# Performance work log

Hardware: AMD Instinct MI355X
Metric: run time of the kernel (lower is better)

## Reference

```python
import jax, jax.numpy as jnp
import numpy as np
from jax import lax

FIELD = 32          # backbone receptive-field stride (field_size of ResNet50)
K = 3               # number of anchor sizes
ANCHOR_PX = (32, 64, 96)
POOL = 2
TILES = 3
NMS_IOU = 0.3
R_POST = 512        # post-NMS proposal cap (static shape for jit)
IMG = 1536
MG = IMG // FIELD   # 48x48 feature map
C = 256
HID = 1024


def setup_inputs() -> dict:
    key = jax.random.key(0)
    ks = jax.random.split(key, 6)
    # create_anchors: per feature cell (grid step FIELD) and per anchor size,
    # row = [x_upper_left, y_upper_left, width, height]
    grid = np.arange(MG, dtype=np.float32) * FIELD + FIELD / 2.0  # cell centers
    cy, cx, aa = np.meshgrid(grid, grid, np.array(ANCHOR_PX, np.float32), indexing='ij')
    anchors = np.stack([cx - aa / 2, cy - aa / 2, aa, aa], axis=-1).reshape(-1, 4).astype(np.float32)
    return {
        'features': jax.random.normal(ks[0], (1, MG, MG, C), jnp.float32),
        'anchors': jnp.asarray(anchors),
        'W_obj': jax.random.normal(ks[1], (C, 2 * K), jnp.float32) * 0.1,
        'b_obj': jnp.zeros((2 * K,), jnp.float32),
        'W_reg': jax.random.normal(ks[2], (C, 4 * K), jnp.float32) * 0.01,
        'b_reg': jnp.zeros((4 * K,), jnp.float32),
        'W_fc1': jax.random.normal(ks[3], (TILES * TILES * C, HID), jnp.float32) * 0.02,
        'b_fc1': jnp.zeros((HID,), jnp.float32),
        'W_fc2': jax.random.normal(ks[4], (HID, 4), jnp.float32) * 0.01,
        'b_fc2': jnp.zeros((4,), jnp.float32),
    }


def _map_outputs(out, anchors):
    # out: [M, N, K*D] RPN output; returns [A, D], one row per anchor
    apx = jnp.asarray(ANCHOR_PX, jnp.int32)
    k = jnp.argmax(anchors[:, 3].astype(jnp.int32)[:, None] == apx[None, :], axis=1)
    px = ((anchors[:, 0] + anchors[:, 2] * 0.5) / FIELD).astype(jnp.int32)
    py = ((anchors[:, 1] + anchors[:, 3] * 0.5) / FIELD).astype(jnp.int32)
    M, N, _ = out.shape
    r = out.reshape(M, N, K, -1)
    return r[py, px, k]


def _unparameterize(reg, anchors):
    cxa = anchors[:, 0] + anchors[:, 2] * 0.5
    cya = anchors[:, 1] + anchors[:, 3] * 0.5
    cx = reg[:, 0] * anchors[:, 2] + cxa
    cy = reg[:, 1] * anchors[:, 3] + cya
    w = anchors[:, 2] * jnp.exp(reg[:, 2])
    h = anchors[:, 3] * jnp.exp(reg[:, 3])
    return jnp.stack([cx - w * 0.5, cy - h * 0.5, w, h], axis=1)


def _clip_boxes(b, W, H):
    x1 = jnp.clip(b[:, 0], 0.0, W)
    y1 = jnp.clip(b[:, 1], 0.0, H)
    x2 = jnp.clip(b[:, 0] + b[:, 2], 0.0, W)
    y2 = jnp.clip(b[:, 1] + b[:, 3], 0.0, H)
    return jnp.stack([x1, y1, x2 - x1, y2 - y1], axis=1)


def _pairwise_iou(b):
    x1, y1 = b[:, 0], b[:, 1]
    x2, y2 = b[:, 0] + b[:, 2], b[:, 1] + b[:, 3]
    iw = jnp.maximum(0.0, jnp.minimum(x2[:, None], x2[None, :]) - jnp.maximum(x1[:, None], x1[None, :]))
    ih = jnp.maximum(0.0, jnp.minimum(y2[:, None], y2[None, :]) - jnp.maximum(y1[:, None], y1[None, :]))
    inter = iw * ih
    area = (x2 - x1) * (y2 - y1)
    return inter / (area[:, None] + area[None, :] - inter + 1e-8)


def _roialign(fmap, boxes):
    # fmap: [M, N, C]; boxes: [R, 4] xywh -> [R, TILES, TILES, C]
    M, N, Cc = fmap.shape
    S = TILES * POOL
    offs = (jnp.arange(S, dtype=boxes.dtype) + 0.5) / S
    fx = jnp.clip((boxes[:, 0:1] + offs[None, :] * boxes[:, 2:3]) / FIELD - 0.5, 0.0, N - 1.0)
    fy = jnp.clip((boxes[:, 1:2] + offs[None, :] * boxes[:, 3:4]) / FIELD - 0.5, 0.0, M - 1.0)
    x0 = jnp.floor(fx).astype(jnp.int32); x1 = jnp.minimum(x0 + 1, N - 1); wx = fx - x0
    y0 = jnp.floor(fy).astype(jnp.int32); y1 = jnp.minimum(y0 + 1, M - 1); wy = fy - y0
    def g(yi, xi):
        return fmap[yi[:, :, None], xi[:, None, :]]  # [R, S, S, C]
    wX = wx[:, None, :, None]; wY = wy[:, :, None, None]
    v = (g(y0, x0) * (1 - wY) * (1 - wX) + g(y0, x1) * (1 - wY) * wX
         + g(y1, x0) * wY * (1 - wX) + g(y1, x1) * wY * wX)
    R = boxes.shape[0]
    return v.reshape(R, TILES, POOL, TILES, POOL, Cc).mean(axis=(2, 4))


def reference(features, anchors, W_obj, b_obj, W_reg, b_reg, W_fc1, b_fc1, W_fc2, b_fc2):
    fmap = features[0]  # [M, N, C]
    out_obj = fmap @ W_obj + b_obj   # [M, N, 2K]
    out_reg = fmap @ W_reg + b_reg   # [M, N, 4K]
    rpn_obj = jax.nn.softmax(_map_outputs(out_obj, anchors), axis=1)  # [A, 2]
    rpn_reg = _map_outputs(out_reg, anchors)                          # [A, 4]
    boxes = _clip_boxes(_unparameterize(rpn_reg, anchors), float(IMG), float(IMG))
    scores = rpn_obj[:, 1]
    A = boxes.shape[0]
    # NMS (sequential greedy suppression on score-sorted boxes)
    order = jnp.argsort(-scores)
    iou_mat = lax.stop_gradient(_pairwise_iou(boxes[order]))  # [A, A], index selection is non-diff
    idx = jnp.arange(A)
    def body(i, keep):
        sup = jnp.any((iou_mat[i] > NMS_IOU) & keep & (idx < i))
        return keep.at[i].set(~sup)
    keep = lax.fori_loop(0, A, body, jnp.zeros((A,), bool))
    masked = jnp.where(keep, scores[order], -1e9)
    _, topi = lax.top_k(masked, R_POST)
    sel = order[topi]
    sel_boxes = boxes[sel]
    sel_obj = rpn_obj[sel]
    pooled = _roialign(fmap, sel_boxes)            # [R, TILES, TILES, C]
    flat = pooled.reshape(R_POST, -1)
    h = jax.nn.relu(flat @ W_fc1 + b_fc1)
    align_reg = h @ W_fc2 + b_fc2                  # [R, 4]
    align_boxes = _unparameterize(align_reg, sel_boxes)
    # concat (rpn_obj, rpn_boxes, align_boxes) -> [R, 10]
    return jnp.concatenate([sel_obj, sel_boxes, align_boxes], axis=1)
```

## Files before the change

kernel.cpp:

```cpp
#include <hip/hip_runtime.h>
#include <hip/hip_bf16.h>

typedef unsigned long long ull;

#define MGRID 48
#define CCH   256
#define NCELL 2304
#define NA    6912
#define NW    108
#define NHID  1024
#define KFC   2304
#define RPOST 512
#define IMGF  1536.0f
#define NQ    5993

typedef __attribute__((ext_vector_type(8))) short short8v;
typedef __attribute__((ext_vector_type(4))) float f32x4;

__global__ __launch_bounds__(256) void rpn_anchor_wcvt(const float* __restrict__ feat,
    const float* __restrict__ Wobj, const float* __restrict__ bobj,
    const float* __restrict__ Wreg, const float* __restrict__ breg,
    const float* __restrict__ anchors, float* __restrict__ probs,
    float* __restrict__ boxes, ull* __restrict__ keys,
    const float* __restrict__ Wfc1, ushort* __restrict__ Wt){
  int t = threadIdx.x;
  if (blockIdx.x >= 192){
    __shared__ float tile[32][33];
    int bid = blockIdx.x - 192;
    int bx = bid & 31;
    int by = bid >> 5;
    int tx = t & 31, ty = t >> 5;
    #pragma unroll
    for (int it=0; it<4; ++it)
      tile[ty + 8*it][tx] = Wfc1[(size_t)(by*32 + ty + 8*it)*NHID + bx*32 + tx];
    __syncthreads();
    #pragma unroll
    for (int it=0; it<4; ++it){
      __hip_bfloat16 b = __float2bfloat16(tile[tx][ty + 8*it]);
      Wt[(size_t)(bx*32 + ty + 8*it)*KFC + by*32 + tx] = *(ushort*)&b;
    }
    return;
  }
  __shared__ float rpn_lds[12*18];
  int cell0 = blockIdx.x * 12;
  if (t < 216){
    int lc = t / 18, o = t % 18;
    const float* W; int stride; float acc;
    if (o < 6){ W = Wobj + o; stride = 6;  acc = bobj[o];   }
    else      { W = Wreg + (o-6); stride = 12; acc = breg[o-6]; }
    const float4* x4 = (const float4*)(feat + (cell0 + lc)*CCH);
    #pragma unroll 4
    for (int c4=0;c4<CCH/4;++c4){
      float4 xv = x4[c4];
      acc += xv.x*W[(4*c4+0)*stride];
      acc += xv.y*W[(4*c4+1)*stride];
      acc += xv.z*W[(4*c4+2)*stride];
      acc += xv.w*W[(4*c4+3)*stride];
    }
    rpn_lds[t] = acc;
  }
  __syncthreads();
  if (t < 36){
    int a = cell0*3 + t;
    int k = t % 3;
    const float* rc = rpn_lds + (t/3)*18;
    float l0 = rc[2*k], l1 = rc[2*k+1];
    float m  = fmaxf(l0,l1);
    float e0 = expf(l0-m), e1 = expf(l1-m);
    float s  = e0 + e1;
    float p0 = e0/s, p1 = e1/s;
    probs[a*2+0] = p0; probs[a*2+1] = p1;
    float4 an = ((const float4*)anchors)[a];
    float r0 = rc[6+4*k+0], r1 = rc[6+4*k+1], r2 = rc[6+4*k+2], r3 = rc[6+4*k+3];
    float cxa = an.x + an.z*0.5f, cya = an.y + an.w*0.5f;
    float cx = r0*an.z + cxa, cy = r1*an.w + cya;
    float w  = an.z*expf(r2),  hh = an.w*expf(r3);
    float bx = cx - w*0.5f, by = cy - hh*0.5f;
    float x1 = fminf(fmaxf(bx,      0.0f), IMGF);
    float y1 = fminf(fmaxf(by,      0.0f), IMGF);
    float x2 = fminf(fmaxf(bx + w,  0.0f), IMGF);
    float y2 = fminf(fmaxf(by + hh, 0.0f), IMGF);
    float4 bo; bo.x = x1; bo.y = y1; bo.z = x2 - x1; bo.w = y2 - y1;
    ((float4*)boxes)[a] = bo;
    keys[a] = ((ull)__float_as_uint(p1) << 32) | (unsigned)(NA-1-a);
  }
}

__global__ __launch_bounds__(256) void rank_part(const ull* __restrict__ keys,
                                                 int* __restrict__ part){
  __shared__ ull lk[256];
  int t = threadIdx.x;
  int ib = blockIdx.x, jb = blockIdx.y;
  lk[t] = keys[jb*256 + t];
  int i = ib*256 + t;
  ull ki = keys[i];
  __syncthreads();
  int cnt = 0;
  #pragma unroll 16
  for (int j=0;j<256;++j) cnt += (lk[j] > ki) ? 1 : 0;
  part[jb*NA + i] = cnt;
}

__global__ __launch_bounds__(256) void rank_scatter(const int* __restrict__ part,
    const float* __restrict__ boxes, int* __restrict__ ord, float* __restrict__ sboxes){
  int i = blockIdx.x*256 + threadIdx.x;
  int r = 0;
  #pragma unroll
  for (int jb=0;jb<27;++jb) r += part[jb*NA + i];
  ord[r] = i;
  ((float4*)sboxes)[r] = ((const float4*)boxes)[i];
}

__global__ __launch_bounds__(256) void iou_mask(const float* __restrict__ sboxes,
                                                ull* __restrict__ maskT){
  int g = blockIdx.x*256 + threadIdx.x;
  int q = g >> 6;
  if (q >= NQ) return;
  int w = (int)((sqrtf(8.0f*(float)q + 9.0f) - 3.0f) * 0.5f);
  if (w > 107) w = 107;
  while (w < 107 && (w+1)*(w+4)/2 <= q) ++w;
  while (w > 0 && w*(w+3)/2 > q) --w;
  int ib = q - w*(w+3)/2;
  int i = ib*64 + (g & 63);
  float4 bi = ((const float4*)sboxes)[i];
  float x1i = bi.x, y1i = bi.y;
  float x2i = bi.x + bi.z, y2i = bi.y + bi.w;
  float ai  = (x2i - x1i) * (y2i - y1i);
  const float4* bj4 = (const float4*)sboxes + w*64;
  ull bits = 0;
  #pragma unroll 8
  for (int jj=0;jj<64;++jj){
    float4 bj = bj4[jj];
    float x1j = bj.x, y1j = bj.y;
    float x2j = bj.x + bj.z, y2j = bj.y + bj.w;
    float aj  = (x2j - x1j) * (y2j - y1j);
    float iw = fmaxf(fminf(x2i,x2j) - fmaxf(x1i,x1j), 0.0f);
    float ih = fmaxf(fminf(y2i,y2j) - fmaxf(y1i,y1j), 0.0f);
    float inter = iw*ih;
    float den = ai + aj - inter + 1e-8f;
    if (inter > 0.3f*den) bits |= (1ull<<jj);
  }
  maskT[(size_t)w*NA + i] = bits;
}

__global__ __launch_bounds__(320) void nms(const ull* __restrict__ maskT,
    const int* __restrict__ ord, const float* __restrict__ sboxes,
    const float* __restrict__ probs, float* __restrict__ out,
    float* __restrict__ selb){
  __shared__ ull remv[NW];
  __shared__ ull keepw[NW];
  __shared__ ull kb_sh[2];
  __shared__ int selpos[RPOST];
  __shared__ int base_sh[NW];
  __shared__ int cnt_sh, done_sh;
  int t = threadIdx.x;
  if (t < NW){ remv[t] = 0ull; keepw[t] = 0ull; }
  if (t == 0){ cnt_sh = 0; done_sh = 0; kb_sh[0] = 0ull; kb_sh[1] = 0ull; }
  __syncthreads();

  ull dg_cur = 0, srow_cur = 0, kb_prev = 0;
  ulonglong2 pre[16];
  #pragma unroll
  for (int b=0;b<16;++b){ pre[b].x = 0ull; pre[b].y = 0ull; }
  if (t < 64) dg_cur = maskT[t];

  const int u  = t - 64;
  const int pw = u >> 1;
  const int h  = u & 1;

  for (int c = 0; c < NW; ++c){
    if (t < 64){
      ull dg_nxt = 0, srow_nxt = 0;
      if (c+1 < NW){
        dg_nxt   = maskT[(size_t)(c+1)*NA + (size_t)(c+1)*64 + t];
        srow_nxt = maskT[(size_t)c*NA + (size_t)(c+1)*64 + t];
      }
      ull w0 = remv[c];
      bool dec  = ((w0 >> t) & 1ull) || ((srow_cur & kb_prev) != 0ull);
      bool kept = false;
      ull sup = dg_cur & ((1ull << t) - 1ull);
      for (;;){
        ull K = __ballot(kept);
        ull D = __ballot(dec);
        if (D == ~0ull) break;
        if (!dec){
          if (sup & K)                 { dec = true; }
          else if ((sup & ~D) == 0ull) { dec = true; kept = true; }
        }
      }
      ull kb = __ballot(kept);
      int cnt0 = cnt_sh;
      ull below = kb & ((1ull << t) - 1ull);
      int myrank = cnt0 + __popcll(below);
      if (kept && myrank < RPOST) selpos[myrank] = c*64 + t;
      if (t == 0){
        kb_sh[c & 1] = kb;
        keepw[c] = kb;
        int nc = cnt0 + __popcll(kb);
        if (nc >= RPOST){ nc = RPOST; done_sh = 1; }
        cnt_sh = nc;
      }
      kb_prev = kb; dg_cur = dg_nxt; srow_cur = srow_nxt;
    } else {
      int wpc = c + 1 + pw;
      if (c >= 1 && wpc < NW){
        ull kbp = kb_sh[(c-1) & 1];
        if (kbp){
          ull acc = 0;
          #pragma unroll
          for (int b=0;b<16;++b){
            acc |= (0ull - ((kbp >> (h*32 + 2*b))   & 1ull)) & pre[b].x;
            acc |= (0ull - ((kbp >> (h*32 + 2*b+1)) & 1ull)) & pre[b].y;
          }
          if (acc) atomicOr(&remv[wpc], acc);
        }
      }
      int wpn = c + 2 + pw;
      if (c+1 < NW && wpn < NW){
        const ulonglong2* src =
          (const ulonglong2*)(maskT + (size_t)wpn*NA + (size_t)c*64) + h*16;
        #pragma unroll
        for (int b=0;b<16;++b) pre[b] = src[b];
      }
    }
    __syncthreads();
    if (done_sh) break;
  }
  __syncthreads();
  int cnt0 = cnt_sh;
  if (cnt0 < RPOST){
    if (t < NW){
      int s = 0;
      for (int w2=0; w2<t; ++w2) s += __popcll(~keepw[w2]);
      base_sh[t] = s;
    }
    __syncthreads();
    for (int p = t; p < NA; p += 320){
      int w2 = p >> 6, b = p & 63;
      ull kw = keepw[w2];
      if (!((kw >> b) & 1ull)){
        int rank = cnt0 + base_sh[w2] + __popcll(~kw & ((1ull << b) - 1ull));
        if (rank < RPOST) selpos[rank] = p;
      }
    }
  }
  __syncthreads();
  for (int s=t; s<RPOST; s+=320){
    int pos = selpos[s];
    int orig = ord[pos];
    float4 b = ((const float4*)sboxes)[pos];
    out[s*10+0] = probs[orig*2+0];
    out[s*10+1] = probs[orig*2+1];
    out[s*10+2] = b.x; out[s*10+3] = b.y; out[s*10+4] = b.z; out[s*10+5] = b.w;
    ((float4*)selb)[s] = b;
  }
}

__global__ __launch_bounds__(256) void roialign(const float* __restrict__ feat,
    const float* __restrict__ selb, __hip_bfloat16* __restrict__ pooled){
  int r = blockIdx.x, c = threadIdx.x;
  float4 b = ((const float4*)selb)[r];
  int x0[6], x1[6], y0[6], y1[6];
  float wx[6], wy[6];
  #pragma unroll
  for (int s=0;s<6;++s){
    float off = ((float)s + 0.5f) / 6.0f;
    float fx = (b.x + off*b.z) / 32.0f - 0.5f;
    fx = fminf(fmaxf(fx, 0.0f), 47.0f);
    int xx0 = (int)floorf(fx);
    x0[s] = xx0; x1[s] = min(xx0+1, 47); wx[s] = fx - (float)xx0;
    float fy = (b.y + off*b.w) / 32.0f - 0.5f;
    fy = fminf(fmaxf(fy, 0.0f), 47.0f);
    int yy0 = (int)floorf(fy);
    y0[s] = yy0; y1[s] = min(yy0+1, 47); wy[s] = fy - (float)yy0;
  }
  #pragma unroll
  for (int ty=0;ty<3;++ty){
    #pragma unroll
    for (int tx=0;tx<3;++tx){
      float sum = 0.0f;
      #pragma unroll
      for (int py=0;py<2;++py){
        #pragma unroll
        for (int px=0;px<2;++px){
          int sy = ty*2+py, sx = tx*2+px;
          float wxx = wx[sx], wyy = wy[sy];
          float v00 = feat[(y0[sy]*MGRID + x0[sx])*CCH + c];
          float v01 = feat[(y0[sy]*MGRID + x1[sx])*CCH + c];
          float v10 = feat[(y1[sy]*MGRID + x0[sx])*CCH + c];
          float v11 = feat[(y1[sy]*MGRID + x1[sx])*CCH + c];
          sum += v00*(1.0f-wyy)*(1.0f-wxx) + v01*(1.0f-wyy)*wxx
               + v10*wyy*(1.0f-wxx)        + v11*wyy*wxx;
        }
      }
      pooled[((r*9) + ty*3 + tx)*CCH + c] = __float2bfloat16(sum * 0.25f);
    }
  }
}

__global__ __launch_bounds__(256) void fc1_mfma(const ushort* __restrict__ A,
    const ushort* __restrict__ Bt, const float* __restrict__ bias,
    float* __restrict__ Hp){
  __shared__ ushort As[4096];
  __shared__ ushort Bs[4096];
  const int t = threadIdx.x;
  const int bn = blockIdx.x, bm = blockIdx.y, bz = blockIdx.z;
  const int wv = t >> 6, lane = t & 63;
  const int wm = (wv >> 1) * 32, wn = (wv & 1) * 32;

  const int r0 = t >> 3, kc = t & 7;
  const int r1 = r0 + 32;
  const int kbase = bz * 144;
  const float4* gA0 = (const float4*)A  + (size_t)(bm*64 + r0)*288 + kbase + kc;
  const float4* gA1 = (const float4*)A  + (size_t)(bm*64 + r1)*288 + kbase + kc;
  const float4* gB0 = (const float4*)Bt + (size_t)(bn*64 + r0)*288 + kbase + kc;
  const float4* gB1 = (const float4*)Bt + (size_t)(bn*64 + r1)*288 + kbase + kc;
  float4* sA0 = (float4*)As + ((r0<<3) | (kc ^ (r0&7)));
  float4* sA1 = (float4*)As + ((r1<<3) | (kc ^ (r1&7)));
  float4* sB0 = (float4*)Bs + ((r0<<3) | (kc ^ (r0&7)));
  float4* sB1 = (float4*)Bs + ((r1<<3) | (kc ^ (r1&7)));

  const int fr = lane & 15, fkg = lane >> 4;
  const int arow0 = wm + fr,      arow1 = wm + 16 + fr;
  const int brow0 = wn + fr,      brow1 = wn + 16 + fr;

  f32x4 acc00{}, acc01{}, acc10{}, acc11{};

  const int KT = 18;
  float4 pa0 = gA0[0], pa1 = gA1[0], pb0 = gB0[0], pb1 = gB1[0];
  for (int kt = 0; kt < KT; ++kt){
    __syncthreads();
    *sA0 = pa0; *sA1 = pa1; *sB0 = pb0; *sB1 = pb1;
    if (kt + 1 < KT){
      pa0 = gA0[(kt+1)*8]; pa1 = gA1[(kt+1)*8];
      pb0 = gB0[(kt+1)*8]; pb1 = gB1[(kt+1)*8];
    }
    __syncthreads();
    #pragma unroll
    for (int kk2 = 0; kk2 < 2; ++kk2){
      int kidx = fkg + kk2*4;
      short8v a0 = *(const short8v*)(As + ((((arow0<<3) | (kidx ^ (arow0&7)))) << 3));
      short8v a1 = *(const short8v*)(As + ((((arow1<<3) | (kidx ^ (arow1&7)))) << 3));
      short8v b0 = *(const short8v*)(Bs + ((((brow0<<3) | (kidx ^ (brow0&7)))) << 3));
      short8v b1 = *(const short8v*)(Bs + ((((brow1<<3) | (kidx ^ (brow1&7)))) << 3));
      acc00 = __builtin_amdgcn_mfma_f32_16x16x32_bf16(a0, b0, acc00, 0, 0, 0);
      acc01 = __builtin_amdgcn_mfma_f32_16x16x32_bf16(a0, b1, acc01, 0, 0, 0);
      acc10 = __builtin_amdgcn_mfma_f32_16x16x32_bf16(a1, b0, acc10, 0, 0, 0);
      acc11 = __builtin_amdgcn_mfma_f32_16x16x32_bf16(a1, b1, acc11, 0, 0, 0);
    }
  }
  float* H = Hp + (size_t)bz * 512 * NHID;
  const int orow = bm*64 + wm + (lane>>4)*4;
  const int ocol = bn*64 + wn + (lane&15);
  #pragma unroll
  for (int i=0;i<2;++i){
    #pragma unroll
    for (int j=0;j<2;++j){
      f32x4 a = (i==0) ? ((j==0)?acc00:acc01) : ((j==0)?acc10:acc11);
      #pragma unroll
      for (int reg=0;reg<4;++reg){
        int row = orow + i*16 + reg;
        int col = ocol + j*16;
        float v = a[reg] + (bz == 0 ? bias[col] : 0.0f);
        H[(size_t)row*NHID + col] = v;
      }
    }
  }
}

__global__ __launch_bounds__(64) void fc2(const float* __restrict__ h0,
    const float* __restrict__ h1, const float* __restrict__ W2,
    const float* __restrict__ b2, const float* __restrict__ selb,
    float* __restrict__ out){
  int r = blockIdx.x, lane = threadIdx.x;
  float a0=0,a1=0,a2=0,a3=0;
  #pragma unroll 4
  for (int it=0; it<16; ++it){
    int k = it*64 + lane;
    float hv = fmaxf(h0[(size_t)r*NHID + k] + h1[(size_t)r*NHID + k], 0.0f);
    float4 w = ((const float4*)W2)[k];
    a0 += hv*w.x; a1 += hv*w.y; a2 += hv*w.z; a3 += hv*w.w;
  }
  #pragma unroll
  for (int off=32; off>0; off>>=1){
    a0 += __shfl_down(a0, off);
    a1 += __shfl_down(a1, off);
    a2 += __shfl_down(a2, off);
    a3 += __shfl_down(a3, off);
  }
  if (lane == 0){
    float4 b = ((const float4*)selb)[r];
    float r0 = a0 + b2[0], r1 = a1 + b2[1], r2 = a2 + b2[2], r3 = a3 + b2[3];
    float cxa = b.x + b.z*0.5f, cya = b.y + b.w*0.5f;
    float cx = r0*b.z + cxa, cy = r1*b.w + cya;
    float w  = b.z*expf(r2),  hh = b.w*expf(r3);
    out[r*10+6] = cx - w*0.5f;
    out[r*10+7] = cy - hh*0.5f;
    out[r*10+8] = w;
    out[r*10+9] = hh;
  }
}

extern "C" void kernel_launch(void* const* d_in, const int* in_sizes, int n_in,
                              void* d_out, int out_size, void* d_ws, size_t ws_size,
                              hipStream_t stream) {
  const float* feat    = (const float*)d_in[0];
  const float* anchors = (const float*)d_in[1];
  const float* Wobj    = (const float*)d_in[2];
  const float* bobj    = (const float*)d_in[3];
  const float* Wreg    = (const float*)d_in[4];
  const float* breg    = (const float*)d_in[5];
  const float* Wfc1    = (const float*)d_in[6];
  const float* bfc1    = (const float*)d_in[7];
  const float* Wfc2    = (const float*)d_in[8];
  const float* bfc2    = (const float*)d_in[9];
  float* out = (float*)d_out;
  char* ws = (char*)d_ws;

  float* probs  = (float*)(ws + 165888);
  float* boxes  = (float*)(ws + 221184);
  ull*   keys   = (ull*)  (ws + 331776);
  int*   ord    = (int*)  (ws + 387072);
  float* sboxes = (float*)(ws + 414720);
  int*   part   = (int*)  (ws + 525312);
  ull*   maskT  = (ull*)  (ws + 1271808);
  float* selb   = (float*)(ws + 7243776);
  __hip_bfloat16* pooled = (__hip_bfloat16*)(ws + 7251968);
  float* h      = (float*)(ws + 9611264);
  ushort* Wt    = (ushort*)(ws + 13805568);

  float* h0 = h;
  float* h1 = h + 512*NHID;

  hipLaunchKernelGGL(rpn_anchor_wcvt, dim3(2496),   dim3(256), 0, stream,
                     feat, Wobj, bobj, Wreg, breg, anchors, probs, boxes, keys, Wfc1, Wt);
  hipLaunchKernelGGL(rank_part,    dim3(27,27),   dim3(256), 0, stream, keys, part);
  hipLaunchKernelGGL(rank_scatter, dim3(27),      dim3(256), 0, stream, part, boxes, ord, sboxes);
  hipLaunchKernelGGL(iou_mask,     dim3(1499),    dim3(256), 0, stream, sboxes, maskT);
  hipLaunchKernelGGL(nms,          dim3(1),       dim3(320), 0, stream, maskT, ord, sboxes, probs, out, selb);
  hipLaunchKernelGGL(roialign,     dim3(512),     dim3(256), 0, stream, feat, selb, pooled);
  hipLaunchKernelGGL(fc1_mfma,     dim3(16,8,2),  dim3(256), 0, stream, (const ushort*)pooled, Wt, bfc1, h);
  hipLaunchKernelGGL(fc2,          dim3(512),     dim3(64),  0, stream, h0, h1, Wfc2, bfc2, selb, out);
}
```

Measured before the change: 88.76 us.

## Process two NMS mask columns per block-sync step in the sequential NMS loop

The single-block NMS now resolves two 64-box chunks per iteration, handling intra-pair suppression with joint ballot loops. This halves the number of __syncthreads rounds, from 108 to 54. The iou_mask triangular indexing is extended so each word column also covers the next chunk, which the paired diagonal needs. In exchange, the worker threads carry twice as many prefetched mask registers, the ballot loop does more work per round, and iou_mask launches slightly more blocks.

Measured after the change: 88.98 us. Within noise of the previous version (+0.2%).

```diff
diff --git a/kernel.cpp b/kernel.cpp
--- a/kernel.cpp
+++ b/kernel.cpp
@@ -8,11 +8,12 @@
 #define NCELL 2304
 #define NA    6912
 #define NW    108
+#define NC    54
 #define NHID  1024
 #define KFC   2304
 #define RPOST 512
 #define IMGF  1536.0f
-#define NQ    5993
+#define NQ2   6204
 
 typedef __attribute__((ext_vector_type(8))) short short8v;
 typedef __attribute__((ext_vector_type(4))) float f32x4;
@@ -111,16 +112,18 @@
   ((float4*)sboxes)[r] = ((const float4*)boxes)[i];
 }
 
+__device__ inline int Gfun(int w){ return (w <= 104) ? (w*(w+7))/2 : 5772 + (w-104)*108; }
 __global__ __launch_bounds__(256) void iou_mask(const float* __restrict__ sboxes,
                                                 ull* __restrict__ maskT){
   int g = blockIdx.x*256 + threadIdx.x;
   int q = g >> 6;
-  if (q >= NQ) return;
-  int w = (int)((sqrtf(8.0f*(float)q + 9.0f) - 3.0f) * 0.5f);
+  if (q >= NQ2) return;
+  int w = (int)((sqrtf(8.0f*(float)q + 49.0f) - 7.0f) * 0.5f);
   if (w > 107) w = 107;
-  while (w < 107 && (w+1)*(w+4)/2 <= q) ++w;
-  while (w > 0 && w*(w+3)/2 > q) --w;
-  int ib = q - w*(w+3)/2;
+  if (w < 0) w = 0;
+  while (w < 107 && Gfun(w+1) <= q) ++w;
+  while (w > 0 && Gfun(w) > q) --w;
+  int ib = q - Gfun(w);
   int i = ib*64 + (g & 63);
   float4 bi = ((const float4*)sboxes)[i];
   float x1i = bi.x, y1i = bi.y;
@@ -149,78 +152,101 @@
     float* __restrict__ selb){
   __shared__ ull remv[NW];
   __shared__ ull keepw[NW];
-  __shared__ ull kb_sh[2];
+  __shared__ ull kb_sh[2][2];
   __shared__ int selpos[RPOST];
   __shared__ int base_sh[NW];
   __shared__ int cnt_sh, done_sh;
   int t = threadIdx.x;
   if (t < NW){ remv[t] = 0ull; keepw[t] = 0ull; }
-  if (t == 0){ cnt_sh = 0; done_sh = 0; kb_sh[0] = 0ull; kb_sh[1] = 0ull; }
+  if (t == 0){ cnt_sh = 0; done_sh = 0;
+               kb_sh[0][0]=0ull; kb_sh[0][1]=0ull; kb_sh[1][0]=0ull; kb_sh[1][1]=0ull; }
   __syncthreads();
 
-  ull dg_cur = 0, srow_cur = 0, kb_prev = 0;
-  ulonglong2 pre[16];
-  #pragma unroll
-  for (int b=0;b<16;++b){ pre[b].x = 0ull; pre[b].y = 0ull; }
-  if (t < 64) dg_cur = maskT[t];
+  ull d00=0, d10=0, d11=0, s0a=0, s0b=0, s1a=0, s1b=0, kbp0=0, kbp1=0;
+  ulonglong2 pre[32];
+  #pragma unroll
+  for (int b=0;b<32;++b){ pre[b].x = 0ull; pre[b].y = 0ull; }
+
+  if (t < 64){
+    d00 = maskT[(size_t)0*NA + t];
+    d10 = maskT[(size_t)0*NA + 64 + t];
+    d11 = maskT[(size_t)1*NA + 64 + t];
+  }
 
   const int u  = t - 64;
   const int pw = u >> 1;
-  const int h  = u & 1;
-
-  for (int c = 0; c < NW; ++c){
+  const int hh = u & 1;
+
+  for (int c = 0; c < NC; ++c){
     if (t < 64){
-      ull dg_nxt = 0, srow_nxt = 0;
-      if (c+1 < NW){
-        dg_nxt   = maskT[(size_t)(c+1)*NA + (size_t)(c+1)*64 + t];
-        srow_nxt = maskT[(size_t)c*NA + (size_t)(c+1)*64 + t];
-      }
-      ull w0 = remv[c];
-      bool dec  = ((w0 >> t) & 1ull) || ((srow_cur & kb_prev) != 0ull);
-      bool kept = false;
-      ull sup = dg_cur & ((1ull << t) - 1ull);
+      ull d00n=0,d10n=0,d11n=0,s0an=0,s0bn=0,s1an=0,s1bn=0;
+      if (c+1 < NC){
+        size_t i0 = (size_t)(c+1)*128 + t;
+        size_t i1 = i0 + 64;
+        d00n = maskT[(size_t)(2*c+2)*NA + i0];
+        d10n = maskT[(size_t)(2*c+2)*NA + i1];
+        d11n = maskT[(size_t)(2*c+3)*NA + i1];
+        s0an = maskT[(size_t)(2*c  )*NA + i0];
+        s0bn = maskT[(size_t)(2*c+1)*NA + i0];
+        s1an = maskT[(size_t)(2*c  )*NA + i1];
+        s1bn = maskT[(size_t)(2*c+1)*NA + i1];
+      }
+      ull w0 = remv[2*c], w1 = remv[2*c+1];
+      bool dec0 = ((w0 >> t) & 1ull) || ((s0a & kbp0) != 0ull) || ((s0b & kbp1) != 0ull);
+      bool dec1 = ((w1 >> t) & 1ull) || ((s1a & kbp0) != 0ull) || ((s1b & kbp1) != 0ull);
+      bool k0 = false, k1 = false;
+      ull below = (1ull << t) - 1ull;
+      ull sup0 = d00 & below;
+      ull sup1 = d11 & below;
       for (;;){
-        ull K = __ballot(kept);
-        ull D = __ballot(dec);
-        if (D == ~0ull) break;
-        if (!dec){
-          if (sup & K)                 { dec = true; }
-          else if ((sup & ~D) == 0ull) { dec = true; kept = true; }
+        ull K0 = __ballot(k0), K1 = __ballot(k1);
+        ull D0 = __ballot(dec0), D1 = __ballot(dec1);
+        if (D0 == ~0ull && D1 == ~0ull) break;
+        if (!dec0){
+          if (sup0 & K0)                 { dec0 = true; }
+          else if ((sup0 & ~D0) == 0ull) { dec0 = true; k0 = true; }
         }
-      }
-      ull kb = __ballot(kept);
+        if (!dec1){
+          if ((d10 & K0) || (sup1 & K1))                       { dec1 = true; }
+          else if (((d10 & ~D0) == 0ull) && ((sup1 & ~D1) == 0ull)) { dec1 = true; k1 = true; }
+        }
+      }
+      ull kb0 = __ballot(k0), kb1 = __ballot(k1);
       int cnt0 = cnt_sh;
-      ull below = kb & ((1ull << t) - 1ull);
-      int myrank = cnt0 + __popcll(below);
-      if (kept && myrank < RPOST) selpos[myrank] = c*64 + t;
+      int r0 = cnt0 + __popcll(kb0 & below);
+      int r1 = cnt0 + __popcll(kb0) + __popcll(kb1 & below);
+      if (k0 && r0 < RPOST) selpos[r0] = c*128 + t;
+      if (k1 && r1 < RPOST) selpos[r1] = c*128 + 64 + t;
       if (t == 0){
-        kb_sh[c & 1] = kb;
-        keepw[c] = kb;
-        int nc = cnt0 + __popcll(kb);
-        if (nc >= RPOST){ nc = RPOST; done_sh = 1; }
-        cnt_sh = nc;
-      }
-      kb_prev = kb; dg_cur = dg_nxt; srow_cur = srow_nxt;
+        kb_sh[c & 1][0] = kb0; kb_sh[c & 1][1] = kb1;
+        keepw[2*c] = kb0; keepw[2*c+1] = kb1;
+        int nc2 = cnt0 + __popcll(kb0) + __popcll(kb1);
+        if (nc2 >= RPOST){ nc2 = RPOST; done_sh = 1; }
+        cnt_sh = nc2;
+      }
+      kbp0 = kb0; kbp1 = kb1;
+      d00 = d00n; d10 = d10n; d11 = d11n;
+      s0a = s0an; s0b = s0bn; s1a = s1an; s1b = s1bn;
     } else {
-      int wpc = c + 1 + pw;
+      int wpc = 2*c + 2 + pw;
       if (c >= 1 && wpc < NW){
-        ull kbp = kb_sh[(c-1) & 1];
+        ull kbp = kb_sh[(c-1) & 1][hh];
         if (kbp){
           ull acc = 0;
           #pragma unroll
-          for (int b=0;b<16;++b){
-            acc |= (0ull - ((kbp >> (h*32 + 2*b))   & 1ull)) & pre[b].x;
-            acc |= (0ull - ((kbp >> (h*32 + 2*b+1)) & 1ull)) & pre[b].y;
+          for (int b=0;b<32;++b){
+            acc |= (0ull - ((kbp >> (2*b))   & 1ull)) & pre[b].x;
+            acc |= (0ull - ((kbp >> (2*b+1)) & 1ull)) & pre[b].y;
           }
           if (acc) atomicOr(&remv[wpc], acc);
         }
       }
-      int wpn = c + 2 + pw;
-      if (c+1 < NW && wpn < NW){
+      int wpn = 2*c + 4 + pw;
+      if (c+1 < NC && wpn < NW){
         const ulonglong2* src =
-          (const ulonglong2*)(maskT + (size_t)wpn*NA + (size_t)c*64) + h*16;
+          (const ulonglong2*)(maskT + (size_t)wpn*NA + (size_t)c*128 + (size_t)hh*64);
         #pragma unroll
-        for (int b=0;b<16;++b) pre[b] = src[b];
+        for (int b=0;b<32;++b) pre[b] = src[b];
       }
     }
     __syncthreads();
@@ -436,7 +462,7 @@
                      feat, Wobj, bobj, Wreg, breg, anchors, probs, boxes, keys, Wfc1, Wt);
   hipLaunchKernelGGL(rank_part,    dim3(27,27),   dim3(256), 0, stream, keys, part);
   hipLaunchKernelGGL(rank_scatter, dim3(27),      dim3(256), 0, stream, part, boxes, ord, sboxes);
-  hipLaunchKernelGGL(iou_mask,     dim3(1499),    dim3(256), 0, stream, sboxes, maskT);
+  hipLaunchKernelGGL(iou_mask,     dim3(1551),    dim3(256), 0, stream, sboxes, maskT);
   hipLaunchKernelGGL(nms,          dim3(1),       dim3(320), 0, stream, maskT, ord, sboxes, probs, out, selb);
   hipLaunchKernelGGL(roialign,     dim3(512),     dim3(256), 0, stream, feat, selb, pooled);
   hipLaunchKernelGGL(fc1_mfma,     dim3(16,8,2),  dim3(256), 0, stream, (const ushort*)pooled, Wt, bfc1, h);
```

## Fuse rank, scatter, IoU mask and NMS into one persistent kernel with atomic flags

Applied to the files above, without the earlier changes.

Merges the rank_part, rank_scatter, iou_mask and nms kernels into one persistent 512-block kernel. Rank partials are summed with packed atomics, and the last contributor scatters each entry. IoU tiles spin-wait on per-chunk completion counters, and block 0 waits for every block before running NMS, now with 256 threads where each helper thread prefetches a whole 64-bit word row. This removes three launch boundaries and the part buffer, at the cost of spin-wait overhead, reliance on all 512 blocks being co-resident, and a larger register array in the NMS helpers.

Result: slower. 304.1 us (+242.5%).

```diff
diff --git a/kernel.cpp b/kernel.cpp
--- a/kernel.cpp
+++ b/kernel.cpp
@@ -13,16 +13,20 @@
 #define RPOST 512
 #define IMGF  1536.0f
 #define NQ    5993
+#define MBLK  512
 
 typedef __attribute__((ext_vector_type(8))) short short8v;
 typedef __attribute__((ext_vector_type(4))) float f32x4;
+
+#define SYNC_WORDS 7021
 
 __global__ __launch_bounds__(256) void rpn_anchor_wcvt(const float* __restrict__ feat,
     const float* __restrict__ Wobj, const float* __restrict__ bobj,
     const float* __restrict__ Wreg, const float* __restrict__ breg,
     const float* __restrict__ anchors, float* __restrict__ probs,
     float* __restrict__ boxes, ull* __restrict__ keys,
-    const float* __restrict__ Wfc1, ushort* __restrict__ Wt){
+    const float* __restrict__ Wfc1, ushort* __restrict__ Wt,
+    unsigned* __restrict__ sync){
   int t = threadIdx.x;
   if (blockIdx.x >= 192){
     __shared__ float tile[32][33];
@@ -40,6 +44,9 @@
       Wt[(size_t)(bx*32 + ty + 8*it)*KFC + by*32 + tx] = *(ushort*)&b;
     }
     return;
+  }
+  if (blockIdx.x == 0){
+    for (int i = t; i < SYNC_WORDS; i += 256) sync[i] = 0u;
   }
   __shared__ float rpn_lds[12*18];
   int cell0 = blockIdx.x * 12;
@@ -86,87 +93,102 @@
   }
 }
 
-__global__ __launch_bounds__(256) void rank_part(const ull* __restrict__ keys,
-                                                 int* __restrict__ part){
+__global__ __launch_bounds__(256, 2) void mid_mega(const ull* __restrict__ keys,
+    const float* __restrict__ boxes, int* __restrict__ ord, float* __restrict__ sboxes,
+    ull* __restrict__ maskT, const float* __restrict__ probs,
+    float* __restrict__ out, float* __restrict__ selb, unsigned* sync){
+  const int bid = blockIdx.x;
+  const int t   = threadIdx.x;
+  unsigned* rank_acc  = sync;
+  unsigned* chunkdone = sync + NA;
+  unsigned* iou_done  = sync + NA + NW;
+
   __shared__ ull lk[256];
-  int t = threadIdx.x;
-  int ib = blockIdx.x, jb = blockIdx.y;
-  lk[t] = keys[jb*256 + t];
-  int i = ib*256 + t;
-  ull ki = keys[i];
-  __syncthreads();
-  int cnt = 0;
-  #pragma unroll 16
-  for (int j=0;j<256;++j) cnt += (lk[j] > ki) ? 1 : 0;
-  part[jb*NA + i] = cnt;
-}
-
-__global__ __launch_bounds__(256) void rank_scatter(const int* __restrict__ part,
-    const float* __restrict__ boxes, int* __restrict__ ord, float* __restrict__ sboxes){
-  int i = blockIdx.x*256 + threadIdx.x;
-  int r = 0;
-  #pragma unroll
-  for (int jb=0;jb<27;++jb) r += part[jb*NA + i];
-  ord[r] = i;
-  ((float4*)sboxes)[r] = ((const float4*)boxes)[i];
-}
-
-__global__ __launch_bounds__(256) void iou_mask(const float* __restrict__ sboxes,
-                                                ull* __restrict__ maskT){
-  int g = blockIdx.x*256 + threadIdx.x;
-  int q = g >> 6;
-  if (q >= NQ) return;
-  int w = (int)((sqrtf(8.0f*(float)q + 9.0f) - 3.0f) * 0.5f);
-  if (w > 107) w = 107;
-  while (w < 107 && (w+1)*(w+4)/2 <= q) ++w;
-  while (w > 0 && w*(w+3)/2 > q) --w;
-  int ib = q - w*(w+3)/2;
-  int i = ib*64 + (g & 63);
-  float4 bi = ((const float4*)sboxes)[i];
-  float x1i = bi.x, y1i = bi.y;
-  float x2i = bi.x + bi.z, y2i = bi.y + bi.w;
-  float ai  = (x2i - x1i) * (y2i - y1i);
-  const float4* bj4 = (const float4*)sboxes + w*64;
-  ull bits = 0;
-  #pragma unroll 8
-  for (int jj=0;jj<64;++jj){
-    float4 bj = bj4[jj];
-    float x1j = bj.x, y1j = bj.y;
-    float x2j = bj.x + bj.z, y2j = bj.y + bj.w;
-    float aj  = (x2j - x1j) * (y2j - y1j);
-    float iw = fmaxf(fminf(x2i,x2j) - fmaxf(x1i,x1j), 0.0f);
-    float ih = fmaxf(fminf(y2i,y2j) - fmaxf(y1i,y1j), 0.0f);
-    float inter = iw*ih;
-    float den = ai + aj - inter + 1e-8f;
-    if (inter > 0.3f*den) bits |= (1ull<<jj);
-  }
-  maskT[(size_t)w*NA + i] = bits;
-}
-
-__global__ __launch_bounds__(320) void nms(const ull* __restrict__ maskT,
-    const int* __restrict__ ord, const float* __restrict__ sboxes,
-    const float* __restrict__ probs, float* __restrict__ out,
-    float* __restrict__ selb){
   __shared__ ull remv[NW];
   __shared__ ull keepw[NW];
   __shared__ ull kb_sh[2];
   __shared__ int selpos[RPOST];
   __shared__ int base_sh[NW];
   __shared__ int cnt_sh, done_sh;
-  int t = threadIdx.x;
+
+  for (int vb = bid; vb < 729; vb += MBLK){
+    int ib = vb % 27, jb = vb / 27;
+    __syncthreads();
+    lk[t] = keys[jb*256 + t];
+    int i = ib*256 + t;
+    ull ki = keys[i];
+    __syncthreads();
+    int cnt = 0;
+    #pragma unroll 16
+    for (int j=0;j<256;++j) cnt += (lk[j] > ki) ? 1 : 0;
+    unsigned old = atomicAdd(&rank_acc[i], (unsigned)cnt | (1u<<16));
+    if ((old >> 16) == 26u){
+      int r = (int)(old & 0xFFFFu) + cnt;
+      ord[r] = i;
+      ((float4*)sboxes)[r] = ((const float4*)boxes)[i];
+      __threadfence();
+      atomicAdd(&chunkdone[r >> 6], 1u);
+    }
+  }
+
+  for (int vb = bid; vb < 1499; vb += MBLK){
+    int g = vb*256 + t;
+    int q = g >> 6;
+    if (q < NQ){
+      int w = (int)((sqrtf(8.0f*(float)q + 9.0f) - 3.0f) * 0.5f);
+      if (w > 107) w = 107;
+      while (w < 107 && (w+1)*(w+4)/2 <= q) ++w;
+      while (w > 0 && w*(w+3)/2 > q) --w;
+      int ib = q - w*(w+3)/2;
+      int i = ib*64 + (g & 63);
+      while (__hip_atomic_load(&chunkdone[w],  __ATOMIC_RELAXED, __HIP_MEMORY_SCOPE_AGENT) < 64u ||
+             __hip_atomic_load(&chunkdone[ib], __ATOMIC_RELAXED, __HIP_MEMORY_SCOPE_AGENT) < 64u)
+        __builtin_amdgcn_s_sleep(1);
+      __threadfence();
+      float4 bi = ((const float4*)sboxes)[i];
+      float x1i = bi.x, y1i = bi.y;
+      float x2i = bi.x + bi.z, y2i = bi.y + bi.w;
+      float ai  = (x2i - x1i) * (y2i - y1i);
+      const float4* bj4 = (const float4*)sboxes + w*64;
+      ull bits = 0;
+      #pragma unroll 8
+      for (int jj=0;jj<64;++jj){
+        float4 bj = bj4[jj];
+        float x1j = bj.x, y1j = bj.y;
+        float x2j = bj.x + bj.z, y2j = bj.y + bj.w;
+        float aj  = (x2j - x1j) * (y2j - y1j);
+        float iw = fmaxf(fminf(x2i,x2j) - fmaxf(x1i,x1j), 0.0f);
+        float ih = fmaxf(fminf(y2i,y2j) - fmaxf(y1i,y1j), 0.0f);
+        float inter = iw*ih;
+        float den = ai + aj - inter + 1e-8f;
+        if (inter > 0.3f*den) bits |= (1ull<<jj);
+      }
+      maskT[(size_t)w*NA + i] = bits;
+    }
+  }
+  __threadfence();
+  __syncthreads();
+  if (t == 0) atomicAdd(iou_done, 1u);
+
+  if (bid != 0) return;
+  if (t == 0){
+    while (__hip_atomic_load(iou_done, __ATOMIC_RELAXED, __HIP_MEMORY_SCOPE_AGENT) < (unsigned)MBLK)
+      __builtin_amdgcn_s_sleep(4);
+  }
+  __syncthreads();
+  __threadfence();
+
   if (t < NW){ remv[t] = 0ull; keepw[t] = 0ull; }
   if (t == 0){ cnt_sh = 0; done_sh = 0; kb_sh[0] = 0ull; kb_sh[1] = 0ull; }
   __syncthreads();
 
   ull dg_cur = 0, srow_cur = 0, kb_prev = 0;
-  ulonglong2 pre[16];
+  ulonglong2 pre[32];
   #pragma unroll
-  for (int b=0;b<16;++b){ pre[b].x = 0ull; pre[b].y = 0ull; }
+  for (int b=0;b<32;++b){ pre[b].x = 0ull; pre[b].y = 0ull; }
   if (t < 64) dg_cur = maskT[t];
 
-  const int u  = t - 64;
-  const int pw = u >> 1;
-  const int h  = u & 1;
+  const int u = t - 64;
 
   for (int c = 0; c < NW; ++c){
     if (t < 64){
@@ -202,25 +224,24 @@
       }
       kb_prev = kb; dg_cur = dg_nxt; srow_cur = srow_nxt;
     } else {
-      int wpc = c + 1 + pw;
+      int wpc = c + 1 + u;
       if (c >= 1 && wpc < NW){
         ull kbp = kb_sh[(c-1) & 1];
         if (kbp){
           ull acc = 0;
           #pragma unroll
-          for (int b=0;b<16;++b){
-            acc |= (0ull - ((kbp >> (h*32 + 2*b))   & 1ull)) & pre[b].x;
-            acc |= (0ull - ((kbp >> (h*32 + 2*b+1)) & 1ull)) & pre[b].y;
+          for (int b=0;b<32;++b){
+            acc |= (0ull - ((kbp >> (2*b))   & 1ull)) & pre[b].x;
+            acc |= (0ull - ((kbp >> (2*b+1)) & 1ull)) & pre[b].y;
           }
           if (acc) atomicOr(&remv[wpc], acc);
         }
       }
-      int wpn = c + 2 + pw;
+      int wpn = c + 2 + u;
       if (c+1 < NW && wpn < NW){
-        const ulonglong2* src =
-          (const ulonglong2*)(maskT + (size_t)wpn*NA + (size_t)c*64) + h*16;
+        const ulonglong2* src = (const ulonglong2*)(maskT + (size_t)wpn*NA + (size_t)c*64);
         #pragma unroll
-        for (int b=0;b<16;++b) pre[b] = src[b];
+        for (int b=0;b<32;++b) pre[b] = src[b];
       }
     }
     __syncthreads();
@@ -235,7 +256,7 @@
       base_sh[t] = s;
     }
     __syncthreads();
-    for (int p = t; p < NA; p += 320){
+    for (int p = t; p < NA; p += 256){
       int w2 = p >> 6, b = p & 63;
       ull kw = keepw[w2];
       if (!((kw >> b) & 1ull)){
@@ -245,7 +266,7 @@
     }
   }
   __syncthreads();
-  for (int s=t; s<RPOST; s+=320){
+  for (int s=t; s<RPOST; s+=256){
     int pos = selpos[s];
     int orig = ord[pos];
     float4 b = ((const float4*)sboxes)[pos];
@@ -422,23 +443,21 @@
   ull*   keys   = (ull*)  (ws + 331776);
   int*   ord    = (int*)  (ws + 387072);
   float* sboxes = (float*)(ws + 414720);
-  int*   part   = (int*)  (ws + 525312);
   ull*   maskT  = (ull*)  (ws + 1271808);
   float* selb   = (float*)(ws + 7243776);
   __hip_bfloat16* pooled = (__hip_bfloat16*)(ws + 7251968);
   float* h      = (float*)(ws + 9611264);
   ushort* Wt    = (ushort*)(ws + 13805568);
+  unsigned* sync= (unsigned*)(ws + 18524160);
 
   float* h0 = h;
   float* h1 = h + 512*NHID;
 
-  hipLaunchKernelGGL(rpn_anchor_wcvt, dim3(2496),   dim3(256), 0, stream,
-                     feat, Wobj, bobj, Wreg, breg, anchors, probs, boxes, keys, Wfc1, Wt);
-  hipLaunchKernelGGL(rank_part,    dim3(27,27),   dim3(256), 0, stream, keys, part);
-  hipLaunchKernelGGL(rank_scatter, dim3(27),      dim3(256), 0, stream, part, boxes, ord, sboxes);
-  hipLaunchKernelGGL(iou_mask,     dim3(1499),    dim3(256), 0, stream, sboxes, maskT);
-  hipLaunchKernelGGL(nms,          dim3(1),       dim3(320), 0, stream, maskT, ord, sboxes, probs, out, selb);
-  hipLaunchKernelGGL(roialign,     dim3(512),     dim3(256), 0, stream, feat, selb, pooled);
-  hipLaunchKernelGGL(fc1_mfma,     dim3(16,8,2),  dim3(256), 0, stream, (const ushort*)pooled, Wt, bfc1, h);
-  hipLaunchKernelGGL(fc2,          dim3(512),     dim3(64),  0, stream, h0, h1, Wfc2, bfc2, selb, out);
-}
+  hipLaunchKernelGGL(rpn_anchor_wcvt, dim3(2496),  dim3(256), 0, stream,
+                     feat, Wobj, bobj, Wreg, breg, anchors, probs, boxes, keys, Wfc1, Wt, sync);
+  hipLaunchKernelGGL(mid_mega,        dim3(MBLK),  dim3(256), 0, stream,
+                     keys, boxes, ord, sboxes, maskT, probs, out, selb, sync);
+  hipLaunchKernelGGL(roialign,        dim3(512),   dim3(256), 0, stream, feat, selb, pooled);
+  hipLaunchKernelGGL(fc1_mfma,        dim3(16,8,2),dim3(256), 0, stream, (const ushort*)pooled, Wt, bfc1, h);
+  hipLaunchKernelGGL(fc2,             dim3(512),   dim3(64),  0, stream, h0, h1, Wfc2, bfc2, selb, out);
+}
```

## Fuse rank kernels via atomic counters and deepen NMS suppression lookahead by one word

Applied to the files above, without the earlier changes.

The rank partial-count and scatter kernels become a single kernel. Each block atomically adds its count plus a completion tag into a per-anchor accumulator, and the last of the 27 contributors scatters the sorted box. This removes one launch and the partial-count buffer round trip. In NMS, the helper warps now fold kept bits two words ahead instead of one. The decision warp checks the two previous words' suppression rows directly, so the helper atomics leave the critical path. The IOU mask grid grows to supply the extra near-diagonal tiles, which adds a little IOU work.

Result: faster. 86.99 us (median of 2 runs) (-2.0%).

```diff
diff --git a/kernel.cpp b/kernel.cpp
--- a/kernel.cpp
+++ b/kernel.cpp
@@ -12,7 +12,7 @@
 #define KFC   2304
 #define RPOST 512
 #define IMGF  1536.0f
-#define NQ    5993
+#define NQ2   6099
 
 typedef __attribute__((ext_vector_type(8))) short short8v;
 typedef __attribute__((ext_vector_type(4))) float f32x4;
@@ -22,7 +22,8 @@
     const float* __restrict__ Wreg, const float* __restrict__ breg,
     const float* __restrict__ anchors, float* __restrict__ probs,
     float* __restrict__ boxes, ull* __restrict__ keys,
-    const float* __restrict__ Wfc1, ushort* __restrict__ Wt){
+    const float* __restrict__ Wfc1, ushort* __restrict__ Wt,
+    unsigned* __restrict__ rank_acc){
   int t = threadIdx.x;
   if (blockIdx.x >= 192){
     __shared__ float tile[32][33];
@@ -40,6 +41,9 @@
       Wt[(size_t)(bx*32 + ty + 8*it)*KFC + by*32 + tx] = *(ushort*)&b;
     }
     return;
+  }
+  if (blockIdx.x == 0){
+    for (int i = t; i < NA; i += 256) rank_acc[i] = 0u;
   }
   __shared__ float rpn_lds[12*18];
   int cell0 = blockIdx.x * 12;
@@ -86,8 +90,9 @@
   }
 }
 
-__global__ __launch_bounds__(256) void rank_part(const ull* __restrict__ keys,
-                                                 int* __restrict__ part){
+__global__ __launch_bounds__(256) void rank_fused(const ull* __restrict__ keys,
+    const float* __restrict__ boxes, unsigned* __restrict__ rank_acc,
+    int* __restrict__ ord, float* __restrict__ sboxes){
   __shared__ ull lk[256];
   int t = threadIdx.x;
   int ib = blockIdx.x, jb = blockIdx.y;
@@ -98,29 +103,26 @@
   int cnt = 0;
   #pragma unroll 16
   for (int j=0;j<256;++j) cnt += (lk[j] > ki) ? 1 : 0;
-  part[jb*NA + i] = cnt;
-}
-
-__global__ __launch_bounds__(256) void rank_scatter(const int* __restrict__ part,
-    const float* __restrict__ boxes, int* __restrict__ ord, float* __restrict__ sboxes){
-  int i = blockIdx.x*256 + threadIdx.x;
-  int r = 0;
-  #pragma unroll
-  for (int jb=0;jb<27;++jb) r += part[jb*NA + i];
-  ord[r] = i;
-  ((float4*)sboxes)[r] = ((const float4*)boxes)[i];
-}
-
+  unsigned old = atomicAdd(&rank_acc[i], (unsigned)cnt | (1u<<16));
+  if ((old >> 16) == 26u){
+    int r = (int)(old & 0xFFFFu) + cnt;
+    ord[r] = i;
+    ((float4*)sboxes)[r] = ((const float4*)boxes)[i];
+  }
+}
+
+__device__ inline int Gfun2(int w){ return (w <= 105) ? (w*(w+5))/2 : 5775 + (w-105)*108; }
 __global__ __launch_bounds__(256) void iou_mask(const float* __restrict__ sboxes,
                                                 ull* __restrict__ maskT){
   int g = blockIdx.x*256 + threadIdx.x;
   int q = g >> 6;
-  if (q >= NQ) return;
-  int w = (int)((sqrtf(8.0f*(float)q + 9.0f) - 3.0f) * 0.5f);
+  if (q >= NQ2) return;
+  int w = (int)((sqrtf(8.0f*(float)q + 25.0f) - 5.0f) * 0.5f);
+  if (w < 0) w = 0;
   if (w > 107) w = 107;
-  while (w < 107 && (w+1)*(w+4)/2 <= q) ++w;
-  while (w > 0 && w*(w+3)/2 > q) --w;
-  int ib = q - w*(w+3)/2;
+  while (w < 107 && Gfun2(w+1) <= q) ++w;
+  while (w > 0 && Gfun2(w) > q) --w;
+  int ib = q - Gfun2(w);
   int i = ib*64 + (g & 63);
   float4 bi = ((const float4*)sboxes)[i];
   float x1i = bi.x, y1i = bi.y;
@@ -158,7 +160,7 @@
   if (t == 0){ cnt_sh = 0; done_sh = 0; kb_sh[0] = 0ull; kb_sh[1] = 0ull; }
   __syncthreads();
 
-  ull dg_cur = 0, srow_cur = 0, kb_prev = 0;
+  ull dg_cur = 0, s1_cur = 0, s2_cur = 0, kbp1 = 0, kbp2 = 0, remv_c = 0;
   ulonglong2 pre[16];
   #pragma unroll
   for (int b=0;b<16;++b){ pre[b].x = 0ull; pre[b].y = 0ull; }
@@ -166,17 +168,19 @@
 
   const int u  = t - 64;
   const int pw = u >> 1;
-  const int h  = u & 1;
+  const int hh = u & 1;
 
   for (int c = 0; c < NW; ++c){
     if (t < 64){
-      ull dg_nxt = 0, srow_nxt = 0;
+      ull dg_n = 0, s1_n = 0, s2_n = 0;
       if (c+1 < NW){
-        dg_nxt   = maskT[(size_t)(c+1)*NA + (size_t)(c+1)*64 + t];
-        srow_nxt = maskT[(size_t)c*NA + (size_t)(c+1)*64 + t];
-      }
-      ull w0 = remv[c];
-      bool dec  = ((w0 >> t) & 1ull) || ((srow_cur & kb_prev) != 0ull);
+        dg_n = maskT[(size_t)(c+1)*NA + (size_t)(c+1)*64 + t];
+        s1_n = maskT[(size_t)c*NA     + (size_t)(c+1)*64 + t];
+        s2_n = (c >= 1) ? maskT[(size_t)(c-1)*NA + (size_t)(c+1)*64 + t] : 0ull;
+      }
+      ull remv_n = (c+1 < NW) ? remv[c+1] : 0ull;
+      bool dec  = ((remv_c >> t) & 1ull) || ((s1_cur & kbp1) != 0ull)
+                                         || ((s2_cur & kbp2) != 0ull);
       bool kept = false;
       ull sup = dg_cur & ((1ull << t) - 1ull);
       for (;;){
@@ -200,25 +204,26 @@
         if (nc >= RPOST){ nc = RPOST; done_sh = 1; }
         cnt_sh = nc;
       }
-      kb_prev = kb; dg_cur = dg_nxt; srow_cur = srow_nxt;
+      kbp2 = kbp1; kbp1 = kb;
+      dg_cur = dg_n; s1_cur = s1_n; s2_cur = s2_n; remv_c = remv_n;
     } else {
-      int wpc = c + 1 + pw;
+      int wpc = c + 2 + pw;
       if (c >= 1 && wpc < NW){
         ull kbp = kb_sh[(c-1) & 1];
         if (kbp){
           ull acc = 0;
           #pragma unroll
           for (int b=0;b<16;++b){
-            acc |= (0ull - ((kbp >> (h*32 + 2*b))   & 1ull)) & pre[b].x;
-            acc |= (0ull - ((kbp >> (h*32 + 2*b+1)) & 1ull)) & pre[b].y;
+            acc |= (0ull - ((kbp >> (hh*32 + 2*b))   & 1ull)) & pre[b].x;
+            acc |= (0ull - ((kbp >> (hh*32 + 2*b+1)) & 1ull)) & pre[b].y;
           }
           if (acc) atomicOr(&remv[wpc], acc);
         }
       }
-      int wpn = c + 2 + pw;
+      int wpn = c + 3 + pw;
       if (c+1 < NW && wpn < NW){
         const ulonglong2* src =
-          (const ulonglong2*)(maskT + (size_t)wpn*NA + (size_t)c*64) + h*16;
+          (const ulonglong2*)(maskT + (size_t)wpn*NA + (size_t)c*64) + hh*16;
         #pragma unroll
         for (int b=0;b<16;++b) pre[b] = src[b];
       }
@@ -422,7 +427,7 @@
   ull*   keys   = (ull*)  (ws + 331776);
   int*   ord    = (int*)  (ws + 387072);
   float* sboxes = (float*)(ws + 414720);
-  int*   part   = (int*)  (ws + 525312);
+  unsigned* rank_acc = (unsigned*)(ws + 525312);
   ull*   maskT  = (ull*)  (ws + 1271808);
   float* selb   = (float*)(ws + 7243776);
   __hip_bfloat16* pooled = (__hip_bfloat16*)(ws + 7251968);
@@ -432,13 +437,12 @@
   float* h0 = h;
   float* h1 = h + 512*NHID;
 
-  hipLaunchKernelGGL(rpn_anchor_wcvt, dim3(2496),   dim3(256), 0, stream,
-                     feat, Wobj, bobj, Wreg, breg, anchors, probs, boxes, keys, Wfc1, Wt);
-  hipLaunchKernelGGL(rank_part,    dim3(27,27),   dim3(256), 0, stream, keys, part);
-  hipLaunchKernelGGL(rank_scatter, dim3(27),      dim3(256), 0, stream, part, boxes, ord, sboxes);
-  hipLaunchKernelGGL(iou_mask,     dim3(1499),    dim3(256), 0, stream, sboxes, maskT);
-  hipLaunchKernelGGL(nms,          dim3(1),       dim3(320), 0, stream, maskT, ord, sboxes, probs, out, selb);
-  hipLaunchKernelGGL(roialign,     dim3(512),     dim3(256), 0, stream, feat, selb, pooled);
-  hipLaunchKernelGGL(fc1_mfma,     dim3(16,8,2),  dim3(256), 0, stream, (const ushort*)pooled, Wt, bfc1, h);
-  hipLaunchKernelGGL(fc2,          dim3(512),     dim3(64),  0, stream, h0, h1, Wfc2, bfc2, selb, out);
-}
+  hipLaunchKernelGGL(rpn_anchor_wcvt, dim3(2496),  dim3(256), 0, stream,
+                     feat, Wobj, bobj, Wreg, breg, anchors, probs, boxes, keys, Wfc1, Wt, rank_acc);
+  hipLaunchKernelGGL(rank_fused,   dim3(27,27),  dim3(256), 0, stream, keys, boxes, rank_acc, ord, sboxes);
+  hipLaunchKernelGGL(iou_mask,     dim3(1525),   dim3(256), 0, stream, sboxes, maskT);
+  hipLaunchKernelGGL(nms,          dim3(1),      dim3(320), 0, stream, maskT, ord, sboxes, probs, out, selb);
+  hipLaunchKernelGGL(roialign,     dim3(512),    dim3(256), 0, stream, feat, selb, pooled);
+  hipLaunchKernelGGL(fc1_mfma,     dim3(16,8,2), dim3(256), 0, stream, (const ushort*)pooled, Wt, bfc1, h);
+  hipLaunchKernelGGL(fc2,          dim3(512),    dim3(64),  0, stream, h0, h1, Wfc2, bfc2, selb, out);
+}
```
